# Performance work log

Measured on AMD Instinct MI355X. Metric: run time of the kernel, lower is better.

## Reference

```python
import jax, jax.numpy as jnp
import numpy as np

N = 50000
E = 1600000
IN_C = 128
HEADS = 4
OUT_C = 16


def setup_inputs() -> dict:
    key = jax.random.key(0)
    ks = jax.random.split(key, 8)
    x = jax.random.normal(ks[0], (N, IN_C), dtype=jnp.float32)
    edge_index = jax.random.randint(ks[1], (2, E), 0, N, dtype=jnp.int64)
    W = jax.random.normal(ks[2], (IN_C, HEADS * OUT_C), dtype=jnp.float32) * (1.0 / np.sqrt(IN_C))
    att_src = jax.random.normal(ks[3], (HEADS, OUT_C), dtype=jnp.float32) * 0.1
    att_dst = jax.random.normal(ks[4], (HEADS, OUT_C), dtype=jnp.float32) * 0.1
    bias_gat = jnp.zeros((HEADS * OUT_C,), dtype=jnp.float32)
    W_out = jax.random.normal(ks[5], (HEADS * OUT_C, 1), dtype=jnp.float32) * (1.0 / np.sqrt(HEADS * OUT_C))
    b_out = jnp.zeros((1,), dtype=jnp.float32)
    return {"x": x, "edge_index": edge_index, "W": W, "att_src": att_src,
            "att_dst": att_dst, "bias_gat": bias_gat, "W_out": W_out, "b_out": b_out}


def reference(x, edge_index, W, att_src, att_dst, bias_gat, W_out, b_out):
    n = x.shape[0]
    # Linear projection, reshape to [N, H, C]
    xw = (x @ W).reshape(n, HEADS, OUT_C)
    # Per-node attention logits: [N, H]
    a_src = jnp.einsum('nhc,hc->nh', xw, att_src)
    a_dst = jnp.einsum('nhc,hc->nh', xw, att_dst)
    src, dst = edge_index[0], edge_index[1]
    # Per-edge raw scores with leaky relu (PyG negative_slope=0.2): [E, H]
    alpha = jax.nn.leaky_relu(a_src[src] + a_dst[dst], negative_slope=0.2)
    # Segment softmax over incoming edges of each destination node
    amax = jax.ops.segment_max(alpha, dst, num_segments=n)  # [N, H]
    ex = jnp.exp(alpha - amax[dst])
    denom = jax.ops.segment_sum(ex, dst, num_segments=n)  # [N, H]
    attn = ex / (denom[dst] + 1e-16)  # [E, H]
    # Weighted scatter-add aggregation: [N, H, C]
    msg = xw[src] * attn[:, :, None]
    agg = jax.ops.segment_sum(msg, dst, num_segments=n)
    out = agg.reshape(n, HEADS * OUT_C) + bias_gat
    out = jax.nn.elu(out)
    y = out @ W_out + b_out  # [N, 1]
    return y.squeeze(-1)
```

## Files before the change

kernel.cpp:

```cpp
#include <hip/hip_runtime.h>
#include <hip/hip_fp16.h>

#define NNODES 50000
#define INC 128
#define HC 64
#define NHEADS 4
#define NBUCK 196
#define NB_A 256
#define PB_CAP 10240
#define PROJ_P 200
#define NTILES 3125
#define WLD 80

typedef _Float16 f16x8 __attribute__((ext_vector_type(8)));
typedef float f32x4 __attribute__((ext_vector_type(4)));

__global__ __launch_bounds__(256) void proj_count_kernel(
    const float* __restrict__ x, const float* __restrict__ W,
    const float* __restrict__ att_s, const float* __restrict__ att_d,
    const int* __restrict__ ei,
    _Float16* __restrict__ xw_h, float* __restrict__ a_src,
    float* __restrict__ a_dst, int* __restrict__ cnt_mat, int E)
{
    __shared__ _Float16 Wh[INC * WLD];
    const int t = threadIdx.x;

    if (blockIdx.x < PROJ_P) {
        if (t < INC) {
            const float* wr = W + t * HC;
            _Float16* dst = Wh + t * WLD;
            float sa0=0,sa1=0,sa2=0,sa3=0, sd0=0,sd1=0,sd2=0,sd3=0;
            #pragma unroll 16
            for (int c = 0; c < 16; ++c) {
                const float w0 = wr[c], w1 = wr[16+c], w2 = wr[32+c], w3 = wr[48+c];
                dst[c] = (_Float16)w0; dst[16+c] = (_Float16)w1;
                dst[32+c] = (_Float16)w2; dst[48+c] = (_Float16)w3;
                sa0 = fmaf(w0, att_s[c],    sa0); sd0 = fmaf(w0, att_d[c],    sd0);
                sa1 = fmaf(w1, att_s[16+c], sa1); sd1 = fmaf(w1, att_d[16+c], sd1);
                sa2 = fmaf(w2, att_s[32+c], sa2); sd2 = fmaf(w2, att_d[32+c], sd2);
                sa3 = fmaf(w3, att_s[48+c], sa3); sd3 = fmaf(w3, att_d[48+c], sd3);
            }
            dst[64] = (_Float16)sa0; dst[65] = (_Float16)sa1;
            dst[66] = (_Float16)sa2; dst[67] = (_Float16)sa3;
            dst[68] = (_Float16)sd0; dst[69] = (_Float16)sd1;
            dst[70] = (_Float16)sd2; dst[71] = (_Float16)sd3;
        }
        __syncthreads();

        const int w = t >> 6, lane = t & 63;
        const int r16 = lane & 15, g = lane >> 4;

        f16x8 bf[5][4];
        #pragma unroll
        for (int ct = 0; ct < 5; ++ct)
            #pragma unroll
            for (int kt = 0; kt < 4; ++kt)
                #pragma unroll
                for (int j = 0; j < 8; ++j)
                    bf[ct][kt][j] = Wh[(kt * 32 + g * 8 + j) * WLD + ct * 16 + r16];

        for (int tile = blockIdx.x * 4 + w; tile < NTILES; tile += PROJ_P * 4) {
            const int n0 = tile * 16;
            const float* xrow = x + (size_t)(n0 + r16) * INC + g * 8;
            f16x8 af[4];
            #pragma unroll
            for (int kt = 0; kt < 4; ++kt) {
                const float4 v0 = *reinterpret_cast<const float4*>(xrow + kt * 32);
                const float4 v1 = *reinterpret_cast<const float4*>(xrow + kt * 32 + 4);
                af[kt][0] = (_Float16)v0.x; af[kt][1] = (_Float16)v0.y;
                af[kt][2] = (_Float16)v0.z; af[kt][3] = (_Float16)v0.w;
                af[kt][4] = (_Float16)v1.x; af[kt][5] = (_Float16)v1.y;
                af[kt][6] = (_Float16)v1.z; af[kt][7] = (_Float16)v1.w;
            }
            f32x4 acc[5];
            #pragma unroll
            for (int ct = 0; ct < 5; ++ct) acc[ct] = (f32x4){0.f, 0.f, 0.f, 0.f};
            #pragma unroll
            for (int ct = 0; ct < 5; ++ct)
                #pragma unroll
                for (int kt = 0; kt < 4; ++kt)
                    acc[ct] = __builtin_amdgcn_mfma_f32_16x16x32_f16(
                        af[kt], bf[ct][kt], acc[ct], 0, 0, 0);

            #pragma unroll
            for (int ct = 0; ct < 4; ++ct)
                #pragma unroll
                for (int r = 0; r < 4; ++r)
                    xw_h[(size_t)(n0 + g * 4 + r) * HC + ct * 16 + r16] =
                        (_Float16)acc[ct][r];
            #pragma unroll
            for (int r = 0; r < 4; ++r) {
                const int n = n0 + g * 4 + r;
                if (r16 < 4)       a_src[n * NHEADS + r16]       = acc[4][r];
                else if (r16 < 8)  a_dst[n * NHEADS + (r16 - 4)] = acc[4][r];
            }
        }
    } else {
        int* lh = (int*)Wh;
        const int blk = blockIdx.x - PROJ_P;
        for (int i = t; i < NBUCK; i += 256) lh[i] = 0;
        __syncthreads();
        const int chunk = (E + NB_A - 1) / NB_A;
        const int beg = blk * chunk;
        const int end = (beg + chunk < E) ? beg + chunk : E;
        for (int i = beg + t; i < end; i += 256)
            atomicAdd(&lh[((unsigned)ei[E + i]) >> 8], 1);
        __syncthreads();
        for (int i = t; i < NBUCK; i += 256)
            cnt_mat[i * NB_A + blk] = lh[i];
    }
}

__global__ __launch_bounds__(1024) void scan_all_kernel(
    const int* __restrict__ cnt_mat, int* __restrict__ offs_mat,
    int* __restrict__ btotal, int* __restrict__ gbase, int E)
{
    __shared__ int sc[1024];
    const int t = threadIdx.x;
    const int CH = (NBUCK * NB_A) / 1024;
    const int base = t * CH;

    int s = 0;
    #pragma unroll 7
    for (int k = 0; k < CH; ++k) s += cnt_mat[base + k];
    sc[t] = s;
    __syncthreads();
    for (int off = 1; off < 1024; off <<= 1) {
        const int u = (t >= off) ? sc[t - off] : 0;
        __syncthreads();
        sc[t] += u;
        __syncthreads();
    }
    int run = sc[t] - s;
    #pragma unroll 7
    for (int k = 0; k < CH; ++k) {
        offs_mat[base + k] = run;
        run += cnt_mat[base + k];
    }
    __syncthreads();
    for (int b = t; b < NBUCK; b += 1024) {
        const int g0 = offs_mat[b * NB_A];
        const int g1 = (b == NBUCK - 1) ? E : offs_mat[(b + 1) * NB_A];
        gbase[b] = g0;
        btotal[b] = g1 - g0;
    }
}

__global__ __launch_bounds__(512) void binA_write(
    const int* __restrict__ ei, const int* __restrict__ offs_mat,
    unsigned* __restrict__ payload, int E)
{
    __shared__ int cur[NBUCK];
    const int t = threadIdx.x, blk = blockIdx.x;
    for (int b = t; b < NBUCK; b += 512)
        cur[b] = offs_mat[b * NB_A + blk];
    __syncthreads();
    const int chunk = (E + NB_A - 1) / NB_A;
    const int beg = blk * chunk;
    const int end = (beg + chunk < E) ? beg + chunk : E;
    for (int i = beg + t; i < end; i += 512) {
        const unsigned s = (unsigned)ei[i];
        const unsigned d = (unsigned)ei[E + i];
        const int pos = atomicAdd(&cur[d >> 8], 1);
        payload[pos] = (s << 16) | d;
    }
}

__global__ __launch_bounds__(512) void passB_kernel(
    const int* __restrict__ btotal, const int* __restrict__ gbase,
    unsigned* __restrict__ payload, int* __restrict__ rowptr)
{
    __shared__ unsigned pl[PB_CAP];
    __shared__ int lh[256];
    __shared__ int sc[256];
    const int b = blockIdx.x, t = threadIdx.x;
    const int base = gbase[b];
    int ecnt = btotal[b]; if (ecnt > PB_CAP) ecnt = PB_CAP;

    for (int i = t; i < ecnt; i += 512) pl[i] = payload[base + i];
    if (t < 256) lh[t] = 0;
    __syncthreads();
    for (int i = t; i < ecnt; i += 512) atomicAdd(&lh[pl[i] & 255], 1);
    __syncthreads();

    const int val = (t < 256) ? lh[t] : 0;
    if (t < 256) sc[t] = val;
    __syncthreads();
    for (int off = 1; off < 256; off <<= 1) {
        const int u = (t >= off && t < 256) ? sc[t - off] : 0;
        __syncthreads();
        if (t < 256) sc[t] += u;
        __syncthreads();
    }
    if (t < 256) {
        const int excl = sc[t] - val;
        const int node = b * 256 + t;
        if (node <= NNODES) rowptr[node] = base + excl;
        lh[t] = excl;
    }
    __syncthreads();

    for (int i = t; i < ecnt; i += 512) {
        const unsigned p = pl[i];
        const int pos = atomicAdd(&lh[p & 255], 1);
        payload[base + pos] = p >> 16;
    }
}

__global__ __launch_bounds__(256) void agg_kernel(
    const int* __restrict__ rowptr, const unsigned* __restrict__ sorted_src,
    const __half* __restrict__ xw_h, const float* __restrict__ a_src,
    const float* __restrict__ a_dst, const float* __restrict__ bias,
    const float* __restrict__ Wo, const float* __restrict__ bo,
    float* __restrict__ y)
{
    const int lane = threadIdx.x & 63;
    const int g = lane >> 3;
    const int q8 = lane & 7;
    const int h = q8 >> 1;
    const int n = blockIdx.x * 4 + (threadIdx.x >> 6);

    const int beg = rowptr[n], end = rowptr[n + 1];
    const float ad = a_dst[n * NHEADS + h];

    float acc[8] = {0.f, 0.f, 0.f, 0.f, 0.f, 0.f, 0.f, 0.f};
    float den = 0.f;
    #pragma unroll 2
    for (int i = beg; i < end; i += 8) {
        const int idx = i + g;
        const int s = (int)sorted_src[idx < end ? idx : end - 1];
        const float av = a_src[s * NHEADS + h] + ad;
        float ex = __expf(fmaxf(av, 0.2f * av));
        if (idx >= end) ex = 0.f;
        if ((q8 & 1) == 0) den += ex;
        const uint4 u = *reinterpret_cast<const uint4*>(xw_h + (size_t)s * HC + q8 * 8);
        const float2 f0 = __half22float2(__builtin_bit_cast(__half2, u.x));
        const float2 f1 = __half22float2(__builtin_bit_cast(__half2, u.y));
        const float2 f2 = __half22float2(__builtin_bit_cast(__half2, u.z));
        const float2 f3 = __half22float2(__builtin_bit_cast(__half2, u.w));
        acc[0] = fmaf(ex, f0.x, acc[0]); acc[1] = fmaf(ex, f0.y, acc[1]);
        acc[2] = fmaf(ex, f1.x, acc[2]); acc[3] = fmaf(ex, f1.y, acc[3]);
        acc[4] = fmaf(ex, f2.x, acc[4]); acc[5] = fmaf(ex, f2.y, acc[5]);
        acc[6] = fmaf(ex, f3.x, acc[6]); acc[7] = fmaf(ex, f3.y, acc[7]);
    }
    #pragma unroll
    for (int off = 8; off <= 32; off <<= 1) {
        #pragma unroll
        for (int j = 0; j < 8; ++j) acc[j] += __shfl_xor(acc[j], off, 64);
        den += __shfl_xor(den, off, 64);
    }
    den += __shfl_xor(den, 1, 64);
    const float inv = 1.f / (den + 1e-16f);
    const float4 bi0 = *reinterpret_cast<const float4*>(&bias[q8 * 8]);
    const float4 bi1 = *reinterpret_cast<const float4*>(&bias[q8 * 8 + 4]);
    const float4 wo0 = *reinterpret_cast<const float4*>(&Wo[q8 * 8]);
    const float4 wo1 = *reinterpret_cast<const float4*>(&Wo[q8 * 8 + 4]);
    const float bis[8] = {bi0.x, bi0.y, bi0.z, bi0.w, bi1.x, bi1.y, bi1.z, bi1.w};
    const float wos[8] = {wo0.x, wo0.y, wo0.z, wo0.w, wo1.x, wo1.y, wo1.z, wo1.w};
    float p = 0.f;
    #pragma unroll
    for (int j = 0; j < 8; ++j) {
        const float v = acc[j] * inv + bis[j];
        p += (v > 0.f ? v : __expf(v) - 1.f) * wos[j];
    }
    p += __shfl_xor(p, 1, 64);
    p += __shfl_xor(p, 2, 64);
    p += __shfl_xor(p, 4, 64);
    if (lane == 0) y[n] = p + bo[0];
}

extern "C" void kernel_launch(void* const* d_in, const int* in_sizes, int n_in,
                              void* d_out, int out_size, void* d_ws, size_t ws_size,
                              hipStream_t stream) {
    const float* x     = (const float*)d_in[0];
    const int*   ei    = (const int*)d_in[1];
    const float* W     = (const float*)d_in[2];
    const float* att_s = (const float*)d_in[3];
    const float* att_d = (const float*)d_in[4];
    const float* bias  = (const float*)d_in[5];
    const float* Wo    = (const float*)d_in[6];
    const float* bo    = (const float*)d_in[7];
    float*       y     = (float*)d_out;

    const int E = in_sizes[1] / 2;

    char* wsb = (char*)d_ws;
    _Float16* xw_h    = (_Float16*)wsb;
    float*    a_src   = (float*)(wsb + 6400000);
    float*    a_dst   = (float*)(wsb + 7200000);
    unsigned* payload = (unsigned*)(wsb + 8000000);
    int*      rowptr  = (int*)(wsb + 14400000);
    int*      cnt_mat = (int*)(wsb + 14600256);
    int*      offs_mat= (int*)(wsb + 14800960);
    int*      btotal  = (int*)(wsb + 15001664);
    int*      gbase   = (int*)(wsb + 15002448);

    proj_count_kernel<<<PROJ_P + NB_A, 256, 0, stream>>>(
        x, W, att_s, att_d, ei, xw_h, a_src, a_dst, cnt_mat, E);
    scan_all_kernel<<<1, 1024, 0, stream>>>(cnt_mat, offs_mat, btotal, gbase, E);
    binA_write<<<NB_A, 512, 0, stream>>>(ei, offs_mat, payload, E);
    passB_kernel<<<NBUCK, 512, 0, stream>>>(btotal, gbase, payload, rowptr);
    agg_kernel<<<NNODES / 4, 256, 0, stream>>>(rowptr, payload,
                                               (const __half*)xw_h, a_src,
                                               a_dst, bias, Wo, bo, y);
}
```

Before: 177.8 us.

## Remove single-block scan kernel by recomputing bucket offsets redundantly per block

```diff
diff --git a/kernel.cpp b/kernel.cpp
--- a/kernel.cpp
+++ b/kernel.cpp
@@ -111,50 +111,40 @@
     }
 }
 
-__global__ __launch_bounds__(1024) void scan_all_kernel(
-    const int* __restrict__ cnt_mat, int* __restrict__ offs_mat,
-    int* __restrict__ btotal, int* __restrict__ gbase, int E)
-{
-    __shared__ int sc[1024];
-    const int t = threadIdx.x;
-    const int CH = (NBUCK * NB_A) / 1024;
-    const int base = t * CH;
-
-    int s = 0;
-    #pragma unroll 7
-    for (int k = 0; k < CH; ++k) s += cnt_mat[base + k];
-    sc[t] = s;
-    __syncthreads();
-    for (int off = 1; off < 1024; off <<= 1) {
-        const int u = (t >= off) ? sc[t - off] : 0;
-        __syncthreads();
-        sc[t] += u;
-        __syncthreads();
-    }
-    int run = sc[t] - s;
-    #pragma unroll 7
-    for (int k = 0; k < CH; ++k) {
-        offs_mat[base + k] = run;
-        run += cnt_mat[base + k];
-    }
-    __syncthreads();
-    for (int b = t; b < NBUCK; b += 1024) {
-        const int g0 = offs_mat[b * NB_A];
-        const int g1 = (b == NBUCK - 1) ? E : offs_mat[(b + 1) * NB_A];
-        gbase[b] = g0;
-        btotal[b] = g1 - g0;
-    }
-}
-
 __global__ __launch_bounds__(512) void binA_write(
-    const int* __restrict__ ei, const int* __restrict__ offs_mat,
+    const int* __restrict__ ei, const int* __restrict__ cnt_mat,
     unsigned* __restrict__ payload, int E)
 {
+    __shared__ int sc[256];
     __shared__ int cur[NBUCK];
     const int t = threadIdx.x, blk = blockIdx.x;
-    for (int b = t; b < NBUCK; b += 512)
-        cur[b] = offs_mat[b * NB_A + blk];
-    __syncthreads();
+
+    int tot = 0, pre = 0;
+    if (t < NBUCK) {
+        const int4* row = (const int4*)(cnt_mat + t * NB_A);
+        #pragma unroll 8
+        for (int k4 = 0; k4 < NB_A / 4; ++k4) {
+            const int4 v = row[k4];
+            tot += v.x + v.y + v.z + v.w;
+        }
+        const int kb = blk >> 2;
+        for (int k4 = 0; k4 < kb; ++k4) {
+            const int4 v = row[k4];
+            pre += v.x + v.y + v.z + v.w;
+        }
+        for (int k = kb * 4; k < blk; ++k) pre += cnt_mat[t * NB_A + k];
+    }
+    if (t < 256) sc[t] = (t < NBUCK) ? tot : 0;
+    __syncthreads();
+    for (int off = 1; off < 256; off <<= 1) {
+        const int u = (t >= off && t < 256) ? sc[t - off] : 0;
+        __syncthreads();
+        if (t < 256) sc[t] += u;
+        __syncthreads();
+    }
+    if (t < NBUCK) cur[t] = (sc[t] - tot) + pre;
+    __syncthreads();
+
     const int chunk = (E + NB_A - 1) / NB_A;
     const int beg = blk * chunk;
     const int end = (beg + chunk < E) ? beg + chunk : E;
@@ -167,15 +157,36 @@
 }
 
 __global__ __launch_bounds__(512) void passB_kernel(
-    const int* __restrict__ btotal, const int* __restrict__ gbase,
-    unsigned* __restrict__ payload, int* __restrict__ rowptr)
+    const int* __restrict__ cnt_mat, unsigned* __restrict__ payload,
+    int* __restrict__ rowptr)
 {
     __shared__ unsigned pl[PB_CAP];
     __shared__ int lh[256];
     __shared__ int sc[256];
+    __shared__ int sbase[2];
     const int b = blockIdx.x, t = threadIdx.x;
-    const int base = gbase[b];
-    int ecnt = btotal[b]; if (ecnt > PB_CAP) ecnt = PB_CAP;
+
+    int tot = 0;
+    if (t < NBUCK) {
+        const int4* row = (const int4*)(cnt_mat + t * NB_A);
+        #pragma unroll 8
+        for (int k4 = 0; k4 < NB_A / 4; ++k4) {
+            const int4 v = row[k4];
+            tot += v.x + v.y + v.z + v.w;
+        }
+    }
+    if (t < 256) sc[t] = (t < NBUCK) ? tot : 0;
+    __syncthreads();
+    for (int off = 1; off < 256; off <<= 1) {
+        const int u = (t >= off && t < 256) ? sc[t - off] : 0;
+        __syncthreads();
+        if (t < 256) sc[t] += u;
+        __syncthreads();
+    }
+    if (t == b) { sbase[0] = sc[t] - tot; sbase[1] = tot; }
+    __syncthreads();
+    const int base = sbase[0];
+    int ecnt = sbase[1]; if (ecnt > PB_CAP) ecnt = PB_CAP;
 
     for (int i = t; i < ecnt; i += 512) pl[i] = payload[base + i];
     if (t < 256) lh[t] = 0;
@@ -225,7 +236,7 @@
 
     float acc[8] = {0.f, 0.f, 0.f, 0.f, 0.f, 0.f, 0.f, 0.f};
     float den = 0.f;
-    #pragma unroll 2
+    #pragma unroll 4
     for (int i = beg; i < end; i += 8) {
         const int idx = i + g;
         const int s = (int)sorted_src[idx < end ? idx : end - 1];
@@ -291,15 +302,11 @@
     unsigned* payload = (unsigned*)(wsb + 8000000);
     int*      rowptr  = (int*)(wsb + 14400000);
     int*      cnt_mat = (int*)(wsb + 14600256);
-    int*      offs_mat= (int*)(wsb + 14800960);
-    int*      btotal  = (int*)(wsb + 15001664);
-    int*      gbase   = (int*)(wsb + 15002448);
 
     proj_count_kernel<<<PROJ_P + NB_A, 256, 0, stream>>>(
         x, W, att_s, att_d, ei, xw_h, a_src, a_dst, cnt_mat, E);
-    scan_all_kernel<<<1, 1024, 0, stream>>>(cnt_mat, offs_mat, btotal, gbase, E);
-    binA_write<<<NB_A, 512, 0, stream>>>(ei, offs_mat, payload, E);
-    passB_kernel<<<NBUCK, 512, 0, stream>>>(btotal, gbase, payload, rowptr);
+    binA_write<<<NB_A, 512, 0, stream>>>(ei, cnt_mat, payload, E);
+    passB_kernel<<<NBUCK, 512, 0, stream>>>(cnt_mat, payload, rowptr);
     agg_kernel<<<NNODES / 4, 256, 0, stream>>>(rowptr, payload,
                                                (const __half*)xw_h, a_src,
                                                a_dst, bias, Wo, bo, y);
```

New measurement: 171.8 us. -3.3%, faster.
